# Kernel optimization log

Measured on AMD Instinct MI355X. Metric: run time of the kernel, lower is better.

The kernel has to match this reference:

```python
import jax, jax.numpy as jnp
import numpy as np

B, T, N = 32, 512, 16
C, V, D, H, L = 150, 832, 512, 512, 5  # chord vocab, note vocab, embed dim, hidden, layers


def setup_inputs() -> dict:
    key = jax.random.key(0)
    ks = jax.random.split(key, 16)
    s = 0.05
    note = jax.random.randint(ks[0], (B, T, N), 0, V)
    chord = jax.random.randint(ks[1], (B, T), 0, C)
    chord_table = jax.random.normal(ks[2], (C, D), jnp.float32) * s
    note_table = jax.random.normal(ks[3], (V, D), jnp.float32) * s
    # GRU layer 0 (input = 2*D), layers 1..L-1 (input = H), gate order r,z,n like torch
    w_ih0 = jax.random.normal(ks[4], (3 * H, 2 * D), jnp.float32) * s
    w_hh0 = jax.random.normal(ks[5], (3 * H, H), jnp.float32) * s
    b_ih0 = jax.random.normal(ks[6], (3 * H,), jnp.float32) * s
    b_hh0 = jax.random.normal(ks[7], (3 * H,), jnp.float32) * s
    w_ih_r = jax.random.normal(ks[8], (L - 1, 3 * H, H), jnp.float32) * s
    w_hh_r = jax.random.normal(ks[9], (L - 1, 3 * H, H), jnp.float32) * s
    b_ih_r = jax.random.normal(ks[10], (L - 1, 3 * H), jnp.float32) * s
    b_hh_r = jax.random.normal(ks[11], (L - 1, 3 * H), jnp.float32) * s
    fc_w = jax.random.normal(ks[12], (C, H), jnp.float32) * s
    fc_b = jax.random.normal(ks[13], (C,), jnp.float32) * s
    return dict(note=note, chord=chord, chord_table=chord_table, note_table=note_table,
                w_ih0=w_ih0, w_hh0=w_hh0, b_ih0=b_ih0, b_hh0=b_hh0,
                w_ih_r=w_ih_r, w_hh_r=w_hh_r, b_ih_r=b_ih_r, b_hh_r=b_hh_r,
                fc_w=fc_w, fc_b=fc_b)


def _gru_layer(x, wih, whh, bih, bhh):
    # x: [B, T, in] -> [B, T, H], torch GRU cell math (gate order r,z,n)
    xp = jnp.einsum('bti,gi->btg', x, wih) + bih          # precompute input proj [B,T,3H]
    xp = jnp.swapaxes(xp, 0, 1)                            # [T,B,3H]
    h0 = jnp.zeros((x.shape[0], whh.shape[1]), x.dtype)

    def step(h, xpt):
        gh = h @ whh.T + bhh
        xr, xz, xn = jnp.split(xpt, 3, axis=-1)
        hr, hz, hn = jnp.split(gh, 3, axis=-1)
        r = jax.nn.sigmoid(xr + hr)
        z = jax.nn.sigmoid(xz + hz)
        n = jnp.tanh(xn + r * hn)
        h_new = (1.0 - z) * n + z * h
        return h_new, h_new

    _, ys = jax.lax.scan(step, h0, xp)
    return jnp.swapaxes(ys, 0, 1)                          # [B,T,H]


def _forward(note, chord, chord_table, note_table, w_ih0, w_hh0, b_ih0, b_hh0,
             w_ih_r, w_hh_r, b_ih_r, b_hh_r, fc_w, fc_b):
    # padding_idx=0: zero row 0 of both tables (also blocks its gradient)
    ct = chord_table.at[0].set(0.0)
    nt = note_table.at[0].set(0.0)
    chord_emb = ct[chord]                                   # [B,T,D]
    # ragged mean over notes before first zero; mask[k]=1 iff no zero in note[...,:k+1]
    mask = jnp.cumprod((note != 0).astype(chord_table.dtype), axis=-1)  # [B,T,N]
    emb = nt[note]                                          # [B,T,N,D]
    cnt = jnp.maximum(mask.sum(-1), 1.0)                    # zero_index==0 case -> mean of zero row
    note_emb = jnp.einsum('btnd,btn->btd', emb, mask) / cnt[..., None]
    x = jnp.concatenate([chord_emb, note_emb], axis=-1)     # [B,T,2D]
    x = _gru_layer(x, w_ih0, w_hh0, b_ih0, b_hh0)
    for l in range(w_ih_r.shape[0]):
        x = _gru_layer(x, w_ih_r[l], w_hh_r[l], b_ih_r[l], b_hh_r[l])
    return x @ fc_w.T + fc_b                                # [B,T,C]


def reference(note, chord, chord_table, note_table, w_ih0, w_hh0, b_ih0, b_hh0,
              w_ih_r, w_hh_r, b_ih_r, b_hh_r, fc_w, fc_b):
    return _forward(note, chord, chord_table, note_table, w_ih0, w_hh0, b_ih0, b_hh0,
                    w_ih_r, w_hh_r, b_ih_r, b_hh_r, fc_w, fc_b)
```

## Files before the change

### kernel.cpp

```cpp
#include <hip/hip_runtime.h>
#include <hip/hip_bf16.h>

#define B_   32
#define T_   512
#define NN_  16
#define CV_  150
#define D_   512
#define H_   512
#define BT_  16384
#define K0_  1024
#define G3H_ 1536
#define NBF_ 160
#define WSZ_ 49152
#define XSLOT_ 16384
#define XRING_ 32
#define HRING_ 8
#define SENT32 0x7f7f7f7fu
#define HCAP 16384
#define XCAP 16384
#define BCAP 65536

using bf16x8 = __attribute__((ext_vector_type(8))) short;
using f32x4  = __attribute__((ext_vector_type(4))) float;
using u32x4  = __attribute__((ext_vector_type(4))) unsigned int;
typedef unsigned long long u64;

__device__ __forceinline__ unsigned short f2bf(float f){
  unsigned int u = __builtin_bit_cast(unsigned int, f);
  u += 0x7fffu + ((u >> 16) & 1u);
  return (unsigned short)(u >> 16);
}

__device__ __forceinline__ void store8(unsigned short* p, f32x4 a, f32x4 b){
  union { unsigned short us[8]; u32x4 v; } u;
  u.us[0]=f2bf(a[0]); u.us[1]=f2bf(a[1]); u.us[2]=f2bf(a[2]); u.us[3]=f2bf(a[3]);
  u.us[4]=f2bf(b[0]); u.us[5]=f2bf(b[1]); u.us[6]=f2bf(b[2]); u.us[7]=f2bf(b[3]);
  *(u32x4*)p = u.v;
}

__device__ __forceinline__ u64 ld_coh_u64(const u64* p){
  return __hip_atomic_load(p, __ATOMIC_RELAXED, __HIP_MEMORY_SCOPE_AGENT);
}
__device__ __forceinline__ void st_coh_u32(void* p, unsigned int v){
  __hip_atomic_store((unsigned int*)p, v, __ATOMIC_RELAXED, __HIP_MEMORY_SCOPE_AGENT);
}
__device__ __forceinline__ void st_flag(int* p, int v){
  __hip_atomic_store(p, v, __ATOMIC_RELAXED, __HIP_MEMORY_SCOPE_AGENT);
}
__device__ __forceinline__ int ld_flag(const int* p){
  return __hip_atomic_load(p, __ATOMIC_RELAXED, __HIP_MEMORY_SCOPE_AGENT);
}

__device__ __forceinline__ bool bad64(u64 q){
  return ((unsigned int)q == SENT32) | ((unsigned int)(q >> 32) == SENT32);
}

__global__ void convert_bf16(const float* __restrict__ src,
                             unsigned short* __restrict__ dst, int n){
  int i = blockIdx.x * 256 + threadIdx.x;
  if (i < n) dst[i] = f2bf(src[i]);
}

__global__ void prep_wfrag(const float* __restrict__ whh0,
                           const float* __restrict__ whhr,
                           const float* __restrict__ wihr,
                           unsigned short* __restrict__ wsw, int total){
  int idx = blockIdx.x * 256 + threadIdx.x;
  if (idx >= total) return;
  int pos = idx & 511;
  int lam = pos >> 3, e = pos & 7;
  int fr  = idx >> 9;
  int ks  = fr & 31;
  int g   = (fr >> 5) % 3;
  int blk = fr / 96;
  int sub = blk & 31, l = blk >> 5;
  int row = g * 512 + sub * 16 + (lam & 15);
  int k   = (ks & 15) * 32 + (lam >> 4) * 8 + e;
  float v;
  if (l == 0) v = (ks < 16) ? whh0[(size_t)row * H_ + k] : 0.f;
  else {
    const float* w = (ks < 16) ? (whhr + (size_t)(l - 1) * G3H_ * H_)
                               : (wihr + (size_t)(l - 1) * G3H_ * H_);
    v = w[(size_t)row * H_ + k];
  }
  wsw[idx] = f2bf(v);
}

__global__ void prep_bias(const float* __restrict__ bhh0,
                          const float* __restrict__ bihr,
                          const float* __restrict__ bhhr,
                          float* __restrict__ bias_sw, int total){
  int idx = blockIdx.x * 256 + threadIdx.x;
  if (idx >= total) return;
  int q = idx & 3, u = (idx >> 2) & 15, sub = (idx >> 6) & 31, l = idx >> 11;
  int j = sub * 16 + u;
  float v;
  if (l == 0){
    v = (q == 0) ? bhh0[j] : (q == 1) ? bhh0[512 + j] : (q == 2) ? 0.f : bhh0[1024 + j];
  } else {
    const float* bi = bihr + (size_t)(l - 1) * G3H_;
    const float* bh = bhhr + (size_t)(l - 1) * G3H_;
    v = (q == 0) ? bi[j] + bh[j]
      : (q == 1) ? bi[512 + j] + bh[512 + j]
      : (q == 2) ? bi[1024 + j] : bh[1024 + j];
  }
  bias_sw[idx] = v;
}

__global__ __launch_bounds__(64) void emb_kernel(
    const int* __restrict__ note, const int* __restrict__ chord,
    const float* __restrict__ ctab, const float* __restrict__ ntab,
    unsigned short* __restrict__ x0){
  const int bt = blockIdx.x;
  const int tid = threadIdx.x;
  __shared__ int sn[NN_];
  if (tid < NN_) sn[tid] = note[bt * NN_ + tid];
  __syncthreads();
  float alive = 1.f, cnt = 0.f;
  float msk[NN_];
  #pragma unroll
  for (int k = 0; k < NN_; ++k){ if (sn[k] == 0) alive = 0.f; msk[k] = alive; cnt += alive; }
  const float inv = 1.f / fmaxf(cnt, 1.f);
  const int ch = chord[bt];
  const int d0 = tid * 8;
  f32x4 c0 = {0.f,0.f,0.f,0.f}, c1 = {0.f,0.f,0.f,0.f};
  if (ch != 0){
    const float* cp = ctab + (size_t)ch * D_ + d0;
    c0 = *(const f32x4*)cp; c1 = *(const f32x4*)(cp + 4);
  }
  f32x4 s0 = {0.f,0.f,0.f,0.f}, s1 = {0.f,0.f,0.f,0.f};
  #pragma unroll
  for (int k = 0; k < NN_; ++k){
    if (msk[k] != 0.f){
      const float* np = ntab + (size_t)sn[k] * D_ + d0;
      s0 += *(const f32x4*)np;
      s1 += *(const f32x4*)(np + 4);
    }
  }
  s0 *= inv; s1 *= inv;
  unsigned short* o = x0 + (size_t)bt * K0_ + d0;
  store8(o, c0, c1);
  store8(o + D_, s0, s1);
}

__global__ __launch_bounds__(256) void gemm_bt(
    const unsigned short* __restrict__ X, const unsigned short* __restrict__ W,
    const float* __restrict__ bias, float* __restrict__ Y,
    int M, int N, int K, int wmode){
  const int lane = threadIdx.x & 63;
  const int wave = threadIdx.x >> 6;
  const int l15 = lane & 15, kq4 = lane >> 4;
  const int m_frag = blockIdx.y * 64 + wave * 16 + l15;
  const int n_base = blockIdx.x * 64;
  f32x4 acc[4] = {{0.f,0.f,0.f,0.f},{0.f,0.f,0.f,0.f},{0.f,0.f,0.f,0.f},{0.f,0.f,0.f,0.f}};
  const unsigned short* xptr = X + (size_t)m_frag * K + kq4 * 8;
  const unsigned short* wptr[4];
  #pragma unroll
  for (int i = 0; i < 4; ++i){
    int n = n_base + i * 16 + l15;
    if (n >= N) n = N - 1;
    wptr[i] = W + (size_t)n * K + kq4 * 8;
  }
  for (int k0 = 0; k0 < K; k0 += 32){
    bf16x8 a = *(const bf16x8*)(xptr + k0);
    #pragma unroll
    for (int i = 0; i < 4; ++i){
      bf16x8 b = *(const bf16x8*)(wptr[i] + k0);
      acc[i] = __builtin_amdgcn_mfma_f32_16x16x32_bf16(a, b, acc[i], 0, 0, 0);
    }
  }
  const int mrow = blockIdx.y * 64 + wave * 16 + kq4 * 4;
  #pragma unroll
  for (int i = 0; i < 4; ++i){
    int n = n_base + i * 16 + l15;
    if (n < N){
      float bv = bias[n];
      #pragma unroll
      for (int r = 0; r < 4; ++r){
        int m = mrow + r;
        float v = acc[i][r] + bv;
        if (wmode == 0) Y[(size_t)m * N + n] = v;
        else            Y[((size_t)(m & (T_-1)) * N + n) * B_ + (m >> 9)] = v;
      }
    }
  }
}

union Ufrag { u64 q[2]; bf16x8 v; };

__global__ __launch_bounds__(256, 1) void gru_fused(
    const float* __restrict__ xp, const unsigned short* __restrict__ wsw,
    const float* __restrict__ bias_sw, unsigned short* hT,
    unsigned short* xT, unsigned short* xout, int* cprog){
  __shared__ unsigned short w_s[96 * 512];
  __shared__ float p_s[2][4][2][2][16][16];

  const int tid = threadIdx.x;
  const int blk = blockIdx.x;
  const int l   = blk >> 5;
  const int sub = blk & 31;

  {
    const u32x4* src = (const u32x4*)(wsw + (size_t)blk * WSZ_);
    u32x4* dst = (u32x4*)w_s;
    #pragma unroll
    for (int i = 0; i < 24; ++i) dst[tid + 256 * i] = src[tid + 256 * i];
  }
  __syncthreads();

  const int lane = tid & 63, wave = tid >> 6;
  const int l15 = lane & 15, l4 = lane >> 4;
  const int myn = wave >> 1;
  const int kh  = wave & 1;
  const int myb = (myn << 4) + l15;
  const int fro = (l4 << 3);
  const int khofs = kh * 256;
  const int khb = kh * 8;

  const int cb = tid & 31;
  const int cj = (tid >> 5) * 2;
  const int jg = sub * 16 + cj;
  const float* bsp = bias_sw + blk * 64;
  const float br0 = bsp[cj*4+0],     bz0 = bsp[cj*4+1],     bx0 = bsp[cj*4+2],     bn0 = bsp[cj*4+3];
  const float br1 = bsp[(cj+1)*4+0], bz1 = bsp[(cj+1)*4+1], bx1 = bsp[(cj+1)*4+2], bn1 = bsp[(cj+1)*4+3];
  float hres0 = 0.f, hres1 = 0.f;

  unsigned short* hTl = hT + (size_t)l * (HRING_ * 32 * 512);
  unsigned short* xTw = xT + (size_t)(l < 4 ? l : 0) * ((size_t)XRING_ * XSLOT_);
  const unsigned short* xTr = xT + (size_t)(l > 0 ? l - 1 : 0) * ((size_t)XRING_ * XSLOT_);
  const int* bp_own = cprog + (l << 5);
  int*       bp_pub = cprog + ((l > 0 ? l - 1 : 0) << 5);

  float era=0,eza=0,ena=0,era1=0,eza1=0,ena1=0;
  float erb=0,ezb=0,enb=0,erb1=0,ezb1=0,enb1=0;
  if (l == 0){
    { const float* xq = xp + (size_t)0 * (G3H_ * B_) + cb;
      era=xq[(size_t)(0*H_+jg)*B_]; era1=xq[(size_t)(0*H_+jg+1)*B_];
      eza=xq[(size_t)(1*H_+jg)*B_]; eza1=xq[(size_t)(1*H_+jg+1)*B_];
      ena=xq[(size_t)(2*H_+jg)*B_]; ena1=xq[(size_t)(2*H_+jg+1)*B_]; }
    { const float* xq = xp + (size_t)1 * (G3H_ * B_) + cb;
      erb=xq[(size_t)(0*H_+jg)*B_]; erb1=xq[(size_t)(0*H_+jg+1)*B_];
      ezb=xq[(size_t)(1*H_+jg)*B_]; ezb1=xq[(size_t)(1*H_+jg+1)*B_];
      enb=xq[(size_t)(2*H_+jg)*B_]; enb1=xq[(size_t)(2*H_+jg+1)*B_]; }
  }

  for (int t = 0; t < T_; ++t){
    const int pb = t & 1;

    Ufrag xb[8];
    const unsigned short* xs = nullptr;
    if (l > 0){
      xs = xTr + (size_t)(t & (XRING_-1)) * XSLOT_ + (size_t)myb * 512 + khofs + fro;
      #pragma unroll
      for (int j = 0; j < 8; ++j){
        const u64* sp = (const u64*)(xs + (j << 5));
        xb[j].q[0] = ld_coh_u64(sp); xb[j].q[1] = ld_coh_u64(sp + 1);
      }
    }

    Ufrag hb[8];
    const unsigned short* hf = hTl + (((size_t)(t & (HRING_-1)) * 32 + myb) << 9) + khofs + fro;
    #pragma unroll
    for (int j = 0; j < 8; ++j){
      const u64* sp = (const u64*)(hf + (j << 5));
      hb[j].q[0] = ld_coh_u64(sp); hb[j].q[1] = ld_coh_u64(sp + 1);
    }

    if (l < 4 && t && (t & 3) == 0){
      int itc = 0;
      while (true){
        int v = (lane < 32) ? ld_flag(&bp_own[lane]) : 0x7fffffff;
        if (__all(v >= t - 4)) break;
        if (++itc > BCAP) break;
        __builtin_amdgcn_s_sleep(2);
      }
    }

    f32x4 accR = {0.f,0.f,0.f,0.f}, accZ = {0.f,0.f,0.f,0.f};
    f32x4 accN = {0.f,0.f,0.f,0.f}, accX = {0.f,0.f,0.f,0.f};

    if (l > 0){
      #pragma unroll
      for (int j = 0; j < 8; ++j){
        int itc = 0;
        while (__any((int)(bad64(xb[j].q[0]) | bad64(xb[j].q[1])))){
          if (++itc > XCAP) break;
          if (itc > 2) __builtin_amdgcn_s_sleep(2);
          const u64* sp = (const u64*)(xs + (j << 5));
          xb[j].q[0] = ld_coh_u64(sp); xb[j].q[1] = ld_coh_u64(sp + 1);
        }
        bf16x8 b  = xb[j].v;
        bf16x8 a0 = *(const bf16x8*)&w_s[(0 * 32 + 16 + khb + j) * 512 + lane * 8];
        bf16x8 a1 = *(const bf16x8*)&w_s[(1 * 32 + 16 + khb + j) * 512 + lane * 8];
        bf16x8 a2 = *(const bf16x8*)&w_s[(2 * 32 + 16 + khb + j) * 512 + lane * 8];
        accR = __builtin_amdgcn_mfma_f32_16x16x32_bf16(a0, b, accR, 0, 0, 0);
        accZ = __builtin_amdgcn_mfma_f32_16x16x32_bf16(a1, b, accZ, 0, 0, 0);
        accX = __builtin_amdgcn_mfma_f32_16x16x32_bf16(a2, b, accX, 0, 0, 0);
      }
    }

    #pragma unroll
    for (int j = 0; j < 8; ++j){
      int itc = 0;
      while (__any((int)(bad64(hb[j].q[0]) | bad64(hb[j].q[1])))){
        if (++itc > HCAP) break;
        if (itc > 2) __builtin_amdgcn_s_sleep(2);
        const u64* sp = (const u64*)(hf + (j << 5));
        hb[j].q[0] = ld_coh_u64(sp); hb[j].q[1] = ld_coh_u64(sp + 1);
      }
      bf16x8 b  = hb[j].v;
      bf16x8 a0 = *(const bf16x8*)&w_s[(0 * 32 + khb + j) * 512 + lane * 8];
      bf16x8 a1 = *(const bf16x8*)&w_s[(1 * 32 + khb + j) * 512 + lane * 8];
      bf16x8 a2 = *(const bf16x8*)&w_s[(2 * 32 + khb + j) * 512 + lane * 8];
      accR = __builtin_amdgcn_mfma_f32_16x16x32_bf16(a0, b, accR, 0, 0, 0);
      accZ = __builtin_amdgcn_mfma_f32_16x16x32_bf16(a1, b, accZ, 0, 0, 0);
      accN = __builtin_amdgcn_mfma_f32_16x16x32_bf16(a2, b, accN, 0, 0, 0);
    }

    float erc=0,ezc=0,enc=0,erc1=0,ezc1=0,enc1=0;
    if (l == 0){
      const float* xq = xp + (size_t)((t + 2) & (T_ - 1)) * (G3H_ * B_) + cb;
      erc=xq[(size_t)(0*H_+jg)*B_]; erc1=xq[(size_t)(0*H_+jg+1)*B_];
      ezc=xq[(size_t)(1*H_+jg)*B_]; ezc1=xq[(size_t)(1*H_+jg+1)*B_];
      enc=xq[(size_t)(2*H_+jg)*B_]; enc1=xq[(size_t)(2*H_+jg+1)*B_];
    }

    #pragma unroll
    for (int r = 0; r < 4; ++r){
      int u = l4 * 4 + r;
      p_s[pb][0][myn][kh][u][l15] = accR[r];
      p_s[pb][1][myn][kh][u][l15] = accZ[r];
      p_s[pb][2][myn][kh][u][l15] = accN[r];
      p_s[pb][3][myn][kh][u][l15] = accX[r];
    }
    __syncthreads();

    {
      const int nt = cb >> 4, bc = cb & 15;
      float rp0 = p_s[pb][0][nt][0][cj][bc]   + p_s[pb][0][nt][1][cj][bc];
      float rp1 = p_s[pb][0][nt][0][cj+1][bc] + p_s[pb][0][nt][1][cj+1][bc];
      float zp0 = p_s[pb][1][nt][0][cj][bc]   + p_s[pb][1][nt][1][cj][bc];
      float zp1 = p_s[pb][1][nt][0][cj+1][bc] + p_s[pb][1][nt][1][cj+1][bc];
      float hp0 = p_s[pb][2][nt][0][cj][bc]   + p_s[pb][2][nt][1][cj][bc];
      float hp1 = p_s[pb][2][nt][0][cj+1][bc] + p_s[pb][2][nt][1][cj+1][bc];
      float xq0 = p_s[pb][3][nt][0][cj][bc]   + p_s[pb][3][nt][1][cj][bc];
      float xq1 = p_s[pb][3][nt][0][cj+1][bc] + p_s[pb][3][nt][1][cj+1][bc];
      float r0 = 1.f / (1.f + __expf(-(rp0 + era  + br0)));
      float r1 = 1.f / (1.f + __expf(-(rp1 + era1 + br1)));
      float z0 = 1.f / (1.f + __expf(-(zp0 + eza  + bz0)));
      float z1 = 1.f / (1.f + __expf(-(zp1 + eza1 + bz1)));
      float nx0 = (l > 0) ? (xq0 + bx0) : ena;
      float nx1 = (l > 0) ? (xq1 + bx1) : ena1;
      float e0 = __expf(2.f * (nx0 + r0 * (hp0 + bn0)));
      float e1 = __expf(2.f * (nx1 + r1 * (hp1 + bn1)));
      float n0 = (e0 - 1.f) / (e0 + 1.f);
      float n1 = (e1 - 1.f) / (e1 + 1.f);
      float h0 = (1.f - z0) * n0 + z0 * hres0; hres0 = h0;
      float h1 = (1.f - z1) * n1 + z1 * hres1; hres1 = h1;
      unsigned int pk = (unsigned int)f2bf(h0) | ((unsigned int)f2bf(h1) << 16);

      st_coh_u32(hTl + (((size_t)((t + 1) & (HRING_-1)) * 32 + cb) << 9) + jg, pk);
      if (l < 4)
        st_coh_u32(xTw + (size_t)(t & (XRING_-1)) * XSLOT_ + (size_t)cb * 512 + jg, pk);
      else
        *(unsigned int*)&xout[((size_t)cb * T_ + t) * H_ + jg] = pk;
      st_coh_u32(hTl + (((size_t)((t + 4) & (HRING_-1)) * 32 + cb) << 9) + jg, SENT32);
      if (l < 4)
        st_coh_u32(xTw + (size_t)((t + 16) & (XRING_-1)) * XSLOT_ + (size_t)cb * 512 + jg, SENT32);

      if (l > 0 && (t & 3) == 3 && tid == 0) st_flag(&bp_pub[sub], t);

      era = erb; eza = ezb; ena = enb; era1 = erb1; eza1 = ezb1; ena1 = enb1;
      erb = erc; ezb = ezc; enb = enc; erb1 = erc1; ezb1 = ezc1; enb1 = enc1;
    }
  }
}

extern "C" void kernel_launch(void* const* d_in, const int* in_sizes, int n_in,
                              void* d_out, int out_size, void* d_ws, size_t ws_size,
                              hipStream_t stream){
  (void)in_sizes; (void)n_in; (void)out_size; (void)ws_size;
  const int*   note  = (const int*)d_in[0];
  const int*   chord = (const int*)d_in[1];
  const float* ctab  = (const float*)d_in[2];
  const float* ntab  = (const float*)d_in[3];
  const float* wih0  = (const float*)d_in[4];
  const float* whh0  = (const float*)d_in[5];
  const float* bih0  = (const float*)d_in[6];
  const float* bhh0  = (const float*)d_in[7];
  const float* wihr  = (const float*)d_in[8];
  const float* whhr  = (const float*)d_in[9];
  const float* bihr  = (const float*)d_in[10];
  const float* bhhr  = (const float*)d_in[11];
  const float* fcw   = (const float*)d_in[12];
  const float* fcb   = (const float*)d_in[13];
  float* out = (float*)d_out;

  char* ws = (char*)d_ws;
  size_t off = 0;
  auto alloc = [&](size_t bytes)->char*{
    char* p = ws + off; off = (off + bytes + 255) & ~(size_t)255; return p;
  };
  int*            cprog   = (int*)alloc(160 * sizeof(int));
  float*          xp      = (float*)alloc((size_t)BT_ * G3H_ * 4);
  unsigned short* wsw     = (unsigned short*)alloc((size_t)NBF_ * WSZ_ * 2);
  float*          bias_sw = (float*)alloc((size_t)NBF_ * 64 * 4);
  unsigned short* fcw_b   = (unsigned short*)alloc((size_t)CV_ * H_ * 2);
  unsigned short* xout    = (unsigned short*)alloc((size_t)BT_ * H_ * 2);
  const size_t hT_bytes = (size_t)5 * HRING_ * 32 * 512 * 2;
  const size_t hT_al    = (hT_bytes + 255) & ~(size_t)255;
  const size_t xT_bytes = (size_t)4 * XRING_ * XSLOT_ * 2;
  const size_t p2_bytes = hT_al + xT_bytes;
  const size_t x0_bytes = (size_t)BT_ * K0_ * 2;
  const size_t x0_al    = (x0_bytes + 255) & ~(size_t)255;
  const size_t p1_bytes = x0_al + (size_t)G3H_ * K0_ * 2;
  char* ovl = alloc(p1_bytes > p2_bytes ? p1_bytes : p2_bytes);
  unsigned short* x0     = (unsigned short*)ovl;
  unsigned short* wih0_b = (unsigned short*)(ovl + x0_al);
  unsigned short* hT     = (unsigned short*)ovl;
  unsigned short* xT     = (unsigned short*)(ovl + hT_al);

  hipMemsetAsync(cprog, 0, 160 * sizeof(int), stream);

  { int n = G3H_ * K0_; convert_bf16<<<(n + 255) / 256, 256, 0, stream>>>(wih0, wih0_b, n); }
  { int n = CV_ * H_;   convert_bf16<<<(n + 255) / 256, 256, 0, stream>>>(fcw, fcw_b, n); }
  { int n = NBF_ * WSZ_;
    prep_wfrag<<<(n + 255) / 256, 256, 0, stream>>>(whh0, whhr, wihr, wsw, n); }
  { int n = NBF_ * 64;
    prep_bias<<<(n + 255) / 256, 256, 0, stream>>>(bhh0, bihr, bhhr, bias_sw, n); }

  emb_kernel<<<BT_, 64, 0, stream>>>(note, chord, ctab, ntab, x0);

  gemm_bt<<<dim3(G3H_ / 64, BT_ / 64), 256, 0, stream>>>(
      x0, wih0_b, bih0, xp, BT_, G3H_, K0_, 1);

  hipMemsetAsync(hT, 0x7F, hT_bytes, stream);
  for (int ll = 0; ll < 5; ++ll)
    hipMemsetAsync(hT + (size_t)ll * (HRING_ * 32 * 512), 0, 32 * 512 * 2, stream);
  hipMemsetAsync(xT, 0x7F, xT_bytes, stream);

  gru_fused<<<NBF_, 256, 0, stream>>>(xp, wsw, bias_sw, hT, xT, xout, cprog);

  gemm_bt<<<dim3((CV_ + 63) / 64, BT_ / 64), 256, 0, stream>>>(
      xout, fcw_b, fcb, out, BT_, CV_, H_, 0);
}
```

Before: 5.741 ms.

## Fuse layer-0 input projection GEMM into persistent GRU kernel with chunk flags

Removes the separate layer-0 input-projection GEMM launch and runs it as extra blocks of the persistent GRU kernel. The GEMM blocks publish 64-timestep chunks through per-chunk progress counters, and layer-0 GRU blocks spin on those counters before reading each chunk, so the projection overlaps the recurrence. The hT/xT ring buffers move into the output buffer so the workspace no longer overlaps them with x0. The risk is that it depends on the 160 GRU blocks being resident while 6144 GEMM blocks are scheduled, and the GEMM blocks use a simple unshared load path that may be slower than the old GEMM.

```diff
diff --git a/kernel.cpp b/kernel.cpp
--- a/kernel.cpp
+++ b/kernel.cpp
@@ -11,6 +11,7 @@
 #define K0_  1024
 #define G3H_ 1536
 #define NBF_ 160
+#define GXB_ 6144
 #define WSZ_ 49152
 #define XSLOT_ 16384
 #define XRING_ 32
@@ -43,6 +44,13 @@
 }
 __device__ __forceinline__ void st_coh_u32(void* p, unsigned int v){
   __hip_atomic_store((unsigned int*)p, v, __ATOMIC_RELAXED, __HIP_MEMORY_SCOPE_AGENT);
+}
+__device__ __forceinline__ float ld_coh_f32(const float* p){
+  return __hip_atomic_load(p, __ATOMIC_RELAXED, __HIP_MEMORY_SCOPE_AGENT);
+}
+__device__ __forceinline__ void st_coh_f32(float* p, float v){
+  __hip_atomic_store((unsigned int*)p, __builtin_bit_cast(unsigned int, v),
+                     __ATOMIC_RELAXED, __HIP_MEMORY_SCOPE_AGENT);
 }
 __device__ __forceinline__ void st_flag(int* p, int v){
   __hip_atomic_store(p, v, __ATOMIC_RELAXED, __HIP_MEMORY_SCOPE_AGENT);
@@ -189,14 +197,62 @@
 union Ufrag { u64 q[2]; bf16x8 v; };
 
 __global__ __launch_bounds__(256, 1) void gru_fused(
-    const float* __restrict__ xp, const unsigned short* __restrict__ wsw,
+    float* xp, const unsigned short* __restrict__ wsw,
     const float* __restrict__ bias_sw, unsigned short* hT,
-    unsigned short* xT, unsigned short* xout, int* cprog){
+    unsigned short* xT, unsigned short* xout, int* cprog,
+    const unsigned short* __restrict__ x0g,
+    const unsigned short* __restrict__ wih0g,
+    const float* __restrict__ bih0g, int* gprog){
   __shared__ unsigned short w_s[96 * 512];
   __shared__ float p_s[2][4][2][2][16][16];
 
   const int tid = threadIdx.x;
   const int blk = blockIdx.x;
+
+  if (blk >= NBF_){
+    const int idx = blk - NBF_;
+    const int gx  = idx % 24;
+    const int gyy = idx / 24;
+    const int bb  = gyy & 31, tc = gyy >> 5;
+    const int m0  = bb * 512 + tc * 64;
+    const int lane = tid & 63, wave = tid >> 6;
+    const int l15 = lane & 15, kq4 = lane >> 4;
+    const int m_frag = m0 + wave * 16 + l15;
+    const int n_base = gx * 64;
+    f32x4 acc[4] = {{0.f,0.f,0.f,0.f},{0.f,0.f,0.f,0.f},{0.f,0.f,0.f,0.f},{0.f,0.f,0.f,0.f}};
+    const unsigned short* xptr = x0g + (size_t)m_frag * K0_ + kq4 * 8;
+    const unsigned short* wptr[4];
+    #pragma unroll
+    for (int i = 0; i < 4; ++i){
+      int n = n_base + i * 16 + l15;
+      wptr[i] = wih0g + (size_t)n * K0_ + kq4 * 8;
+    }
+    for (int k0 = 0; k0 < K0_; k0 += 32){
+      bf16x8 a = *(const bf16x8*)(xptr + k0);
+      #pragma unroll
+      for (int i = 0; i < 4; ++i){
+        bf16x8 b = *(const bf16x8*)(wptr[i] + k0);
+        acc[i] = __builtin_amdgcn_mfma_f32_16x16x32_bf16(a, b, acc[i], 0, 0, 0);
+      }
+    }
+    const int mrow = m0 + wave * 16 + kq4 * 4;
+    #pragma unroll
+    for (int i = 0; i < 4; ++i){
+      int n = n_base + i * 16 + l15;
+      float bv = bih0g[n];
+      #pragma unroll
+      for (int r = 0; r < 4; ++r){
+        int m = mrow + r;
+        float v = acc[i][r] + bv;
+        st_coh_f32(&xp[((size_t)(m & (T_-1)) * G3H_ + n) * B_ + (m >> 9)], v);
+      }
+    }
+    asm volatile("s_waitcnt vmcnt(0)" ::: "memory");
+    __syncthreads();
+    if (tid == 0) atomicAdd(&gprog[tc], 1);
+    return;
+  }
+
   const int l   = blk >> 5;
   const int sub = blk & 31;
 
@@ -234,14 +290,22 @@
   float era=0,eza=0,ena=0,era1=0,eza1=0,ena1=0;
   float erb=0,ezb=0,enb=0,erb1=0,ezb1=0,enb1=0;
   if (l == 0){
+    if (tid == 0){
+      int itc = 0;
+      while (ld_flag(&gprog[0]) < 768){
+        if (++itc > (1 << 24)) break;
+        __builtin_amdgcn_s_sleep(8);
+      }
+    }
+    __syncthreads();
     { const float* xq = xp + (size_t)0 * (G3H_ * B_) + cb;
-      era=xq[(size_t)(0*H_+jg)*B_]; era1=xq[(size_t)(0*H_+jg+1)*B_];
-      eza=xq[(size_t)(1*H_+jg)*B_]; eza1=xq[(size_t)(1*H_+jg+1)*B_];
-      ena=xq[(size_t)(2*H_+jg)*B_]; ena1=xq[(size_t)(2*H_+jg+1)*B_]; }
+      era=ld_coh_f32(&xq[(size_t)(0*H_+jg)*B_]); era1=ld_coh_f32(&xq[(size_t)(0*H_+jg+1)*B_]);
+      eza=ld_coh_f32(&xq[(size_t)(1*H_+jg)*B_]); eza1=ld_coh_f32(&xq[(size_t)(1*H_+jg+1)*B_]);
+      ena=ld_coh_f32(&xq[(size_t)(2*H_+jg)*B_]); ena1=ld_coh_f32(&xq[(size_t)(2*H_+jg+1)*B_]); }
     { const float* xq = xp + (size_t)1 * (G3H_ * B_) + cb;
-      erb=xq[(size_t)(0*H_+jg)*B_]; erb1=xq[(size_t)(0*H_+jg+1)*B_];
-      ezb=xq[(size_t)(1*H_+jg)*B_]; ezb1=xq[(size_t)(1*H_+jg+1)*B_];
-      enb=xq[(size_t)(2*H_+jg)*B_]; enb1=xq[(size_t)(2*H_+jg+1)*B_]; }
+      erb=ld_coh_f32(&xq[(size_t)(0*H_+jg)*B_]); erb1=ld_coh_f32(&xq[(size_t)(0*H_+jg+1)*B_]);
+      ezb=ld_coh_f32(&xq[(size_t)(1*H_+jg)*B_]); ezb1=ld_coh_f32(&xq[(size_t)(1*H_+jg+1)*B_]);
+      enb=ld_coh_f32(&xq[(size_t)(2*H_+jg)*B_]); enb1=ld_coh_f32(&xq[(size_t)(2*H_+jg+1)*B_]); }
   }
 
   for (int t = 0; t < T_; ++t){
@@ -266,7 +330,15 @@
       hb[j].q[0] = ld_coh_u64(sp); hb[j].q[1] = ld_coh_u64(sp + 1);
     }
 
-    if (l < 4 && t && (t & 3) == 0){
+    if (l < 4 && l > 0 && t && (t & 3) == 0){
+      int itc = 0;
+      while (true){
+        int v = (lane < 32) ? ld_flag(&bp_own[lane]) : 0x7fffffff;
+        if (__all(v >= t - 4)) break;
+        if (++itc > BCAP) break;
+        __builtin_amdgcn_s_sleep(2);
+      }
+    } else if (l == 0 && t && (t & 3) == 0){
       int itc = 0;
       while (true){
         int v = (lane < 32) ? ld_flag(&bp_own[lane]) : 0x7fffffff;
@@ -319,10 +391,21 @@
 
     float erc=0,ezc=0,enc=0,erc1=0,ezc1=0,enc1=0;
     if (l == 0){
+      if (((t + 2) & 63) == 0){
+        const int ck = ((t + 2) & (T_ - 1)) >> 6;
+        if (tid == 0){
+          int itc = 0;
+          while (ld_flag(&gprog[ck]) < 768){
+            if (++itc > (1 << 24)) break;
+            __builtin_amdgcn_s_sleep(8);
+          }
+        }
+        __syncthreads();
+      }
       const float* xq = xp + (size_t)((t + 2) & (T_ - 1)) * (G3H_ * B_) + cb;
-      erc=xq[(size_t)(0*H_+jg)*B_]; erc1=xq[(size_t)(0*H_+jg+1)*B_];
-      ezc=xq[(size_t)(1*H_+jg)*B_]; ezc1=xq[(size_t)(1*H_+jg+1)*B_];
-      enc=xq[(size_t)(2*H_+jg)*B_]; enc1=xq[(size_t)(2*H_+jg+1)*B_];
+      erc=ld_coh_f32(&xq[(size_t)(0*H_+jg)*B_]); erc1=ld_coh_f32(&xq[(size_t)(0*H_+jg+1)*B_]);
+      ezc=ld_coh_f32(&xq[(size_t)(1*H_+jg)*B_]); ezc1=ld_coh_f32(&xq[(size_t)(1*H_+jg+1)*B_]);
+      enc=ld_coh_f32(&xq[(size_t)(2*H_+jg)*B_]); enc1=ld_coh_f32(&xq[(size_t)(2*H_+jg+1)*B_]);
     }
 
     #pragma unroll
@@ -402,25 +485,27 @@
     char* p = ws + off; off = (off + bytes + 255) & ~(size_t)255; return p;
   };
   int*            cprog   = (int*)alloc(160 * sizeof(int));
+  int*            gprog   = (int*)alloc(8 * sizeof(int));
   float*          xp      = (float*)alloc((size_t)BT_ * G3H_ * 4);
   unsigned short* wsw     = (unsigned short*)alloc((size_t)NBF_ * WSZ_ * 2);
   float*          bias_sw = (float*)alloc((size_t)NBF_ * 64 * 4);
   unsigned short* fcw_b   = (unsigned short*)alloc((size_t)CV_ * H_ * 2);
   unsigned short* xout    = (unsigned short*)alloc((size_t)BT_ * H_ * 2);
+  unsigned short* x0      = (unsigned short*)alloc((size_t)BT_ * K0_ * 2);
+  unsigned short* wih0_b  = (unsigned short*)alloc((size_t)G3H_ * K0_ * 2);
+
   const size_t hT_bytes = (size_t)5 * HRING_ * 32 * 512 * 2;
   const size_t hT_al    = (hT_bytes + 255) & ~(size_t)255;
   const size_t xT_bytes = (size_t)4 * XRING_ * XSLOT_ * 2;
-  const size_t p2_bytes = hT_al + xT_bytes;
-  const size_t x0_bytes = (size_t)BT_ * K0_ * 2;
-  const size_t x0_al    = (x0_bytes + 255) & ~(size_t)255;
-  const size_t p1_bytes = x0_al + (size_t)G3H_ * K0_ * 2;
-  char* ovl = alloc(p1_bytes > p2_bytes ? p1_bytes : p2_bytes);
-  unsigned short* x0     = (unsigned short*)ovl;
-  unsigned short* wih0_b = (unsigned short*)(ovl + x0_al);
-  unsigned short* hT     = (unsigned short*)ovl;
-  unsigned short* xT     = (unsigned short*)(ovl + hT_al);
+  unsigned short* hT = (unsigned short*)d_out;
+  unsigned short* xT = (unsigned short*)((char*)d_out + hT_al);
 
   hipMemsetAsync(cprog, 0, 160 * sizeof(int), stream);
+  hipMemsetAsync(gprog, 0, 8 * sizeof(int), stream);
+  hipMemsetAsync(hT, 0x7F, hT_bytes, stream);
+  for (int ll = 0; ll < 5; ++ll)
+    hipMemsetAsync(hT + (size_t)ll * (HRING_ * 32 * 512), 0, 32 * 512 * 2, stream);
+  hipMemsetAsync(xT, 0x7F, xT_bytes, stream);
 
   { int n = G3H_ * K0_; convert_bf16<<<(n + 255) / 256, 256, 0, stream>>>(wih0, wih0_b, n); }
   { int n = CV_ * H_;   convert_bf16<<<(n + 255) / 256, 256, 0, stream>>>(fcw, fcw_b, n); }
@@ -431,15 +516,8 @@
 
   emb_kernel<<<BT_, 64, 0, stream>>>(note, chord, ctab, ntab, x0);
 
-  gemm_bt<<<dim3(G3H_ / 64, BT_ / 64), 256, 0, stream>>>(
-      x0, wih0_b, bih0, xp, BT_, G3H_, K0_, 1);
-
-  hipMemsetAsync(hT, 0x7F, hT_bytes, stream);
-  for (int ll = 0; ll < 5; ++ll)
-    hipMemsetAsync(hT + (size_t)ll * (HRING_ * 32 * 512), 0, 32 * 512 * 2, stream);
-  hipMemsetAsync(xT, 0x7F, xT_bytes, stream);
-
-  gru_fused<<<NBF_, 256, 0, stream>>>(xp, wsw, bias_sw, hT, xT, xout, cprog);
+  gru_fused<<<NBF_ + GXB_, 256, 0, stream>>>(xp, wsw, bias_sw, hT, xT, xout, cprog,
+                                             x0, wih0_b, bih0, gprog);
 
   gemm_bt<<<dim3((CV_ + 63) / 64, BT_ / 64), 256, 0, stream>>>(
       xout, fcw_b, fcb, out, BT_, CV_, H_, 0);
```

New measurement: 5.318 ms. -7.4%, faster.
